# Kernel optimization log

Measured on AMD Instinct MI355X. Metric: run time of the kernel, lower is better.

Reference implementation:

```python
import jax, jax.numpy as jnp
import numpy as np

DIM = 64        # output embedding dim
N_CHUNKS = 3
D = 4           # per-core dim = ceil(DIM ** (1/N_CHUNKS))
RANK = 16
HRANGE = 131072
BATCH = 131072


def setup_inputs() -> dict:
    key = jax.random.key(0)
    k_hs, k_s, k_e, k_c = jax.random.split(key, 4)
    hs = jax.random.randint(k_hs, (BATCH, N_CHUNKS), 0, HRANGE, dtype=jnp.int64)
    # init per reset_parameters (split_dim=True): scale = (d*rank)**-0.5 for cores/end,
    # start_core uniform in +-d**-0.5
    scale = (D * RANK) ** -0.5
    s0 = D ** -0.5
    start_core = jax.random.uniform(k_s, (HRANGE, D, RANK), jnp.float32, -s0, s0)
    end_core = jax.random.uniform(k_e, (HRANGE, D, RANK), jnp.float32, -scale, scale)
    cores = jax.random.uniform(k_c, (N_CHUNKS - 2, HRANGE, D, RANK, RANK), jnp.float32, -scale, scale)
    return {"hs": hs, "start_core": start_core, "end_core": end_core, "cores": cores}


def reference(hs, start_core, end_core, cores):
    B = hs.shape[0]
    # split_dim=True branch of TensorTrainEmbedding.forward
    v = end_core[hs[:, -1]]                      # [B, d, r]
    for i in range(hs.shape[1] - 2):             # fixed small loop over TT cores
        core = cores[i][hs[:, i + 1]]            # [B, d, r, r] irregular gather
        v = jnp.einsum('bdsr,ber->bdes', core, v)  # [B, d, e, r]
        v = v.reshape(B, -1, v.shape[-1])        # flatten(1,2) -> [B, d*e, r]
    v = jnp.einsum('bdr,ber->bde', start_core[hs[:, 0]], v)  # [B, d, e]
    v = v.reshape(B, -1)[:, :DIM]                # [B, dim]
    return v
```

## Files before the change

### kernel.cpp

```cpp
#include <hip/hip_runtime.h>


#define CAP 16
#define WPB 4
#define T_STRIDE 20
#define HRANGE_C 131072

#define WS_COUNTS_OFF 0
#define WS_TABLE_OFF  (HRANGE_C * 4)
#define WS_NEEDED     (HRANGE_C * 4 + HRANGE_C * CAP * 4)

#define WAVE_LDS_FENCE() do { \
    asm volatile("s_waitcnt lgkmcnt(0)" ::: "memory"); \
    __builtin_amdgcn_sched_barrier(0); \
} while (0)

__global__ __launch_bounds__(256) void build_kernel(
    const int* __restrict__ hs, unsigned* __restrict__ counts,
    unsigned* __restrict__ table, int B)
{
    int b = blockIdx.x * 256 + threadIdx.x;
    if (b < B) {
        unsigned h1 = (unsigned)hs[3 * b + 1];
        unsigned slot = atomicAdd(&counts[h1], 1u);
        if (slot < CAP) table[h1 * CAP + slot] = (unsigned)b;
    }
}

__global__ __launch_bounds__(256) void tt_embed_dedup_kernel(
    const int* __restrict__ hs,
    const float* __restrict__ start_core,
    const float* __restrict__ end_core,
    const float* __restrict__ cores,
    const unsigned* __restrict__ counts,
    const unsigned* __restrict__ table,
    float* __restrict__ out)
{
    __shared__ __align__(16) float lds_t[WPB][16 * T_STRIDE];

    const int tid  = threadIdx.x;
    const int wave = tid >> 6;
    const int lane = tid & 63;

    int bin = blockIdx.x * WPB + wave;
    bin = __builtin_amdgcn_readfirstlane(bin);

    int cnt = (int)counts[bin];
    cnt = __builtin_amdgcn_readfirstlane(cnt);
    if (cnt == 0) return;
    if (cnt > CAP) cnt = CAP;

    const float* crp = cores + ((size_t)bin << 10) + lane * 16;
    float c[16];
    *(float4*)(c + 0)  = *(const float4*)(crp + 0);
    *(float4*)(c + 4)  = *(const float4*)(crp + 4);
    *(float4*)(c + 8)  = *(const float4*)(crp + 8);
    *(float4*)(c + 12) = *(const float4*)(crp + 12);

    const int d = lane >> 4;
    const int s = lane & 15;
    float* tw = &lds_t[wave][(d * 4) * T_STRIDE + s];
    const float* tr = &lds_t[wave][(lane & 15) * T_STRIDE];

    for (int j = 0; j < cnt; ++j) {
        int b = (int)table[bin * CAP + j];
        b = __builtin_amdgcn_readfirstlane(b);
        const int h0 = __builtin_amdgcn_readfirstlane(hs[3 * b + 0]);
        const int h2 = __builtin_amdgcn_readfirstlane(hs[3 * b + 2]);

        const float* stp = start_core + ((size_t)h0 << 6) + ((lane >> 4) << 4);
        float st[16];
        *(float4*)(st + 0)  = *(const float4*)(stp + 0);
        *(float4*)(st + 4)  = *(const float4*)(stp + 4);
        *(float4*)(st + 8)  = *(const float4*)(stp + 8);
        *(float4*)(st + 12) = *(const float4*)(stp + 12);

        const float* v0p = end_core + ((size_t)h2 << 6);
        #pragma unroll
        for (int e = 0; e < 4; ++e) {
            const float* ve = v0p + e * 16;
            float a = c[0] * ve[0];
            #pragma unroll
            for (int r = 1; r < 16; ++r)
                a = fmaf(c[r], ve[r], a);
            tw[e * T_STRIDE] = a;
        }

        WAVE_LDS_FENCE();

        float tt[16];
        *(float4*)(tt + 0)  = *(const float4*)(tr + 0);
        *(float4*)(tt + 4)  = *(const float4*)(tr + 4);
        *(float4*)(tt + 8)  = *(const float4*)(tr + 8);
        *(float4*)(tt + 12) = *(const float4*)(tr + 12);

        float a = st[0] * tt[0];
        #pragma unroll
        for (int k = 1; k < 16; ++k)
            a = fmaf(st[k], tt[k], a);

        out[((size_t)b << 6) + lane] = a;

        WAVE_LDS_FENCE();
    }
}

__global__ __launch_bounds__(256) void tt_embed_plain_kernel(
    const int* __restrict__ hs,
    const float* __restrict__ start_core,
    const float* __restrict__ end_core,
    const float* __restrict__ cores,
    float* __restrict__ out,
    int B)
{
    __shared__ __align__(16) float lds_t[WPB][16 * T_STRIDE];
    const int tid  = threadIdx.x;
    const int wave = tid >> 6;
    const int lane = tid & 63;

    int b = blockIdx.x * WPB + wave;
    b = __builtin_amdgcn_readfirstlane(b);
    if (b >= B) return;

    const int h0 = __builtin_amdgcn_readfirstlane(hs[3 * b + 0]);
    const int h1 = __builtin_amdgcn_readfirstlane(hs[3 * b + 1]);
    const int h2 = __builtin_amdgcn_readfirstlane(hs[3 * b + 2]);

    const float* crp = cores + ((size_t)h1 << 10) + lane * 16;
    float c[16];
    *(float4*)(c + 0)  = *(const float4*)(crp + 0);
    *(float4*)(c + 4)  = *(const float4*)(crp + 4);
    *(float4*)(c + 8)  = *(const float4*)(crp + 8);
    *(float4*)(c + 12) = *(const float4*)(crp + 12);

    const float* stp = start_core + ((size_t)h0 << 6) + ((lane >> 4) << 4);
    float st[16];
    *(float4*)(st + 0)  = *(const float4*)(stp + 0);
    *(float4*)(st + 4)  = *(const float4*)(stp + 4);
    *(float4*)(st + 8)  = *(const float4*)(stp + 8);
    *(float4*)(st + 12) = *(const float4*)(stp + 12);

    const float* v0p = end_core + ((size_t)h2 << 6);
    const int d = lane >> 4;
    const int s = lane & 15;
    #pragma unroll
    for (int e = 0; e < 4; ++e) {
        const float* ve = v0p + e * 16;
        float a = c[0] * ve[0];
        #pragma unroll
        for (int r = 1; r < 16; ++r)
            a = fmaf(c[r], ve[r], a);
        lds_t[wave][(d * 4 + e) * T_STRIDE + s] = a;
    }

    WAVE_LDS_FENCE();

    const float* tp = &lds_t[wave][(lane & 15) * T_STRIDE];
    float tt[16];
    *(float4*)(tt + 0)  = *(const float4*)(tp + 0);
    *(float4*)(tt + 4)  = *(const float4*)(tp + 4);
    *(float4*)(tt + 8)  = *(const float4*)(tp + 8);
    *(float4*)(tt + 12) = *(const float4*)(tp + 12);

    float a = st[0] * tt[0];
    #pragma unroll
    for (int k = 1; k < 16; ++k)
        a = fmaf(st[k], tt[k], a);
    out[((size_t)b << 6) + lane] = a;
}

extern "C" void kernel_launch(void* const* d_in, const int* in_sizes, int n_in,
                              void* d_out, int out_size, void* d_ws, size_t ws_size,
                              hipStream_t stream) {
    const int*   hs         = (const int*)d_in[0];
    const float* start_core = (const float*)d_in[1];
    const float* end_core   = (const float*)d_in[2];
    const float* cores      = (const float*)d_in[3];
    float* out = (float*)d_out;

    const int B = in_sizes[0] / 3;

    const bool dedup = (B == HRANGE_C) && (ws_size >= (size_t)WS_NEEDED);

    if (dedup) {
        unsigned* counts = (unsigned*)((char*)d_ws + WS_COUNTS_OFF);
        unsigned* table  = (unsigned*)((char*)d_ws + WS_TABLE_OFF);

        hipMemsetAsync(counts, 0, HRANGE_C * 4, stream);
        hipLaunchKernelGGL(build_kernel, dim3((B + 255) / 256), dim3(256), 0,
                           stream, hs, counts, table, B);
        hipLaunchKernelGGL(tt_embed_dedup_kernel,
                           dim3(HRANGE_C / WPB), dim3(256), 0, stream,
                           hs, start_core, end_core, cores, counts, table, out);
    } else {
        hipLaunchKernelGGL(tt_embed_plain_kernel,
                           dim3((B + WPB - 1) / WPB), dim3(256), 0, stream,
                           hs, start_core, end_core, cores, out, B);
    }
}
```

Baseline: 108.7 us.

## Compact non-empty bins into a worklist and add an overflow path

The build step now stores h0 and h2 next to the batch index in uint4 table entries, so the main kernel no longer rereads hs. A compaction kernel builds a worklist of only the non-empty h1 bins, and a grid-stride main kernel walks that list instead of launching one wave per possible bin, many of which are empty. CAP drops to 8, and entries past it go to an overflow list that a separate small kernel processes, so no rows are silently dropped. The cost is two extra kernel launches and more atomics on shared counters.

```diff
diff --git a/kernel.cpp b/kernel.cpp
--- a/kernel.cpp
+++ b/kernel.cpp
@@ -1,14 +1,19 @@
 #include <hip/hip_runtime.h>
 
 
-#define CAP 16
+#define CAP 8
 #define WPB 4
 #define T_STRIDE 20
 #define HRANGE_C 131072
+#define MAIN_BLOCKS 8192
+#define OVF_BLOCKS 32
 
 #define WS_COUNTS_OFF 0
-#define WS_TABLE_OFF  (HRANGE_C * 4)
-#define WS_NEEDED     (HRANGE_C * 4 + HRANGE_C * CAP * 4)
+#define WS_CTRS_OFF   (HRANGE_C * 4)
+#define WS_WORK_OFF   (1u << 20)
+#define WS_OVF_OFF    ((1u << 20) + (HRANGE_C * 4))
+#define WS_TABLE_OFF  (2u << 20)
+#define WS_NEEDED     ((2u << 20) + (size_t)HRANGE_C * CAP * 16)
 
 #define WAVE_LDS_FENCE() do { \
     asm volatile("s_waitcnt lgkmcnt(0)" ::: "memory"); \
@@ -17,56 +22,146 @@
 
 __global__ __launch_bounds__(256) void build_kernel(
     const int* __restrict__ hs, unsigned* __restrict__ counts,
-    unsigned* __restrict__ table, int B)
+    uint4* __restrict__ table, unsigned* __restrict__ ctrs,
+    unsigned* __restrict__ ovf, int B)
 {
     int b = blockIdx.x * 256 + threadIdx.x;
-    if (b < B) {
-        unsigned h1 = (unsigned)hs[3 * b + 1];
-        unsigned slot = atomicAdd(&counts[h1], 1u);
-        if (slot < CAP) table[h1 * CAP + slot] = (unsigned)b;
-    }
-}
-
-__global__ __launch_bounds__(256) void tt_embed_dedup_kernel(
+    if (b >= B) return;
+    unsigned h0 = (unsigned)hs[3 * b + 0];
+    unsigned h1 = (unsigned)hs[3 * b + 1];
+    unsigned h2 = (unsigned)hs[3 * b + 2];
+    unsigned slot = atomicAdd(&counts[h1], 1u);
+    if (slot < CAP) {
+        table[h1 * CAP + slot] = make_uint4((unsigned)b, h0, h2, 0u);
+    } else {
+        unsigned o = atomicAdd(&ctrs[1], 1u);
+        ovf[o] = (unsigned)b;
+    }
+}
+
+__global__ __launch_bounds__(256) void compact_kernel(
+    const unsigned* __restrict__ counts, unsigned* __restrict__ ctrs,
+    unsigned* __restrict__ worklist)
+{
+    int h = blockIdx.x * 256 + threadIdx.x;
+    unsigned c = counts[h];
+    if (c > 0) {
+        unsigned cc = c > CAP ? (unsigned)CAP : c;
+        unsigned s = atomicAdd(&ctrs[0], 1u);
+        worklist[s] = (unsigned)h | (cc << 20);
+    }
+}
+
+__global__ __launch_bounds__(256) void tt_main_kernel(
+    const float* __restrict__ start_core,
+    const float* __restrict__ end_core,
+    const float* __restrict__ cores,
+    const unsigned* __restrict__ ctrs,
+    const unsigned* __restrict__ worklist,
+    const uint4* __restrict__ table,
+    float* __restrict__ out)
+{
+    __shared__ __align__(16) float lds_t[WPB][16 * T_STRIDE];
+
+    const int tid  = threadIdx.x;
+    const int wave = tid >> 6;
+    const int lane = tid & 63;
+
+    const int n = __builtin_amdgcn_readfirstlane((int)ctrs[0]);
+    const int stride = MAIN_BLOCKS * WPB;
+
+    const int d = lane >> 4;
+    const int s = lane & 15;
+    float* tw = &lds_t[wave][(d * 4) * T_STRIDE + s];
+    const float* tr = &lds_t[wave][(lane & 15) * T_STRIDE];
+
+    for (int i = blockIdx.x * WPB + wave; i < n; i += stride) {
+        const unsigned w = (unsigned)__builtin_amdgcn_readfirstlane(
+                               (int)worklist[i]);
+        const int h1  = (int)(w & 0xFFFFFu);
+        const int cnt = (int)(w >> 20);
+
+        const float* crp = cores + ((size_t)h1 << 10) + lane * 16;
+        float c[16];
+        *(float4*)(c + 0)  = *(const float4*)(crp + 0);
+        *(float4*)(c + 4)  = *(const float4*)(crp + 4);
+        *(float4*)(c + 8)  = *(const float4*)(crp + 8);
+        *(float4*)(c + 12) = *(const float4*)(crp + 12);
+
+        const uint4* ep = table + (size_t)h1 * CAP;
+
+        for (int j = 0; j < cnt; ++j) {
+            const uint4 e = ep[j];
+            const int b  = __builtin_amdgcn_readfirstlane((int)e.x);
+            const int h0 = __builtin_amdgcn_readfirstlane((int)e.y);
+            const int h2 = __builtin_amdgcn_readfirstlane((int)e.z);
+
+            const float* stp = start_core + ((size_t)h0 << 6) + ((lane >> 4) << 4);
+            float st[16];
+            *(float4*)(st + 0)  = *(const float4*)(stp + 0);
+            *(float4*)(st + 4)  = *(const float4*)(stp + 4);
+            *(float4*)(st + 8)  = *(const float4*)(stp + 8);
+            *(float4*)(st + 12) = *(const float4*)(stp + 12);
+
+            const float* v0p = end_core + ((size_t)h2 << 6);
+            #pragma unroll
+            for (int e4 = 0; e4 < 4; ++e4) {
+                const float* ve = v0p + e4 * 16;
+                float a = c[0] * ve[0];
+                #pragma unroll
+                for (int r = 1; r < 16; ++r)
+                    a = fmaf(c[r], ve[r], a);
+                tw[e4 * T_STRIDE] = a;
+            }
+
+            WAVE_LDS_FENCE();
+
+            float tt[16];
+            *(float4*)(tt + 0)  = *(const float4*)(tr + 0);
+            *(float4*)(tt + 4)  = *(const float4*)(tr + 4);
+            *(float4*)(tt + 8)  = *(const float4*)(tr + 8);
+            *(float4*)(tt + 12) = *(const float4*)(tr + 12);
+
+            float a = st[0] * tt[0];
+            #pragma unroll
+            for (int k = 1; k < 16; ++k)
+                a = fmaf(st[k], tt[k], a);
+
+            out[((size_t)b << 6) + lane] = a;
+
+            WAVE_LDS_FENCE();
+        }
+    }
+}
+
+__global__ __launch_bounds__(256) void tt_ovf_kernel(
     const int* __restrict__ hs,
     const float* __restrict__ start_core,
     const float* __restrict__ end_core,
     const float* __restrict__ cores,
-    const unsigned* __restrict__ counts,
-    const unsigned* __restrict__ table,
+    const unsigned* __restrict__ ctrs,
+    const unsigned* __restrict__ ovf,
     float* __restrict__ out)
 {
     __shared__ __align__(16) float lds_t[WPB][16 * T_STRIDE];
-
     const int tid  = threadIdx.x;
     const int wave = tid >> 6;
     const int lane = tid & 63;
 
-    int bin = blockIdx.x * WPB + wave;
-    bin = __builtin_amdgcn_readfirstlane(bin);
-
-    int cnt = (int)counts[bin];
-    cnt = __builtin_amdgcn_readfirstlane(cnt);
-    if (cnt == 0) return;
-    if (cnt > CAP) cnt = CAP;
-
-    const float* crp = cores + ((size_t)bin << 10) + lane * 16;
-    float c[16];
-    *(float4*)(c + 0)  = *(const float4*)(crp + 0);
-    *(float4*)(c + 4)  = *(const float4*)(crp + 4);
-    *(float4*)(c + 8)  = *(const float4*)(crp + 8);
-    *(float4*)(c + 12) = *(const float4*)(crp + 12);
-
-    const int d = lane >> 4;
-    const int s = lane & 15;
-    float* tw = &lds_t[wave][(d * 4) * T_STRIDE + s];
-    const float* tr = &lds_t[wave][(lane & 15) * T_STRIDE];
-
-    for (int j = 0; j < cnt; ++j) {
-        int b = (int)table[bin * CAP + j];
-        b = __builtin_amdgcn_readfirstlane(b);
+    const int nv = __builtin_amdgcn_readfirstlane((int)ctrs[1]);
+
+    for (int k = blockIdx.x * WPB + wave; k < nv; k += OVF_BLOCKS * WPB) {
+        const int b  = __builtin_amdgcn_readfirstlane((int)ovf[k]);
         const int h0 = __builtin_amdgcn_readfirstlane(hs[3 * b + 0]);
+        const int h1 = __builtin_amdgcn_readfirstlane(hs[3 * b + 1]);
         const int h2 = __builtin_amdgcn_readfirstlane(hs[3 * b + 2]);
+
+        const float* crp = cores + ((size_t)h1 << 10) + lane * 16;
+        float c[16];
+        *(float4*)(c + 0)  = *(const float4*)(crp + 0);
+        *(float4*)(c + 4)  = *(const float4*)(crp + 4);
+        *(float4*)(c + 8)  = *(const float4*)(crp + 8);
+        *(float4*)(c + 12) = *(const float4*)(crp + 12);
 
         const float* stp = start_core + ((size_t)h0 << 6) + ((lane >> 4) << 4);
         float st[16];
@@ -76,36 +171,38 @@
         *(float4*)(st + 12) = *(const float4*)(stp + 12);
 
         const float* v0p = end_core + ((size_t)h2 << 6);
+        const int d = lane >> 4;
+        const int s = lane & 15;
         #pragma unroll
-        for (int e = 0; e < 4; ++e) {
-            const float* ve = v0p + e * 16;
+        for (int e4 = 0; e4 < 4; ++e4) {
+            const float* ve = v0p + e4 * 16;
             float a = c[0] * ve[0];
             #pragma unroll
             for (int r = 1; r < 16; ++r)
                 a = fmaf(c[r], ve[r], a);
-            tw[e * T_STRIDE] = a;
+            lds_t[wave][(d * 4 + e4) * T_STRIDE + s] = a;
         }
 
         WAVE_LDS_FENCE();
 
+        const float* tp = &lds_t[wave][(lane & 15) * T_STRIDE];
         float tt[16];
-        *(float4*)(tt + 0)  = *(const float4*)(tr + 0);
-        *(float4*)(tt + 4)  = *(const float4*)(tr + 4);
-        *(float4*)(tt + 8)  = *(const float4*)(tr + 8);
-        *(float4*)(tt + 12) = *(const float4*)(tr + 12);
+        *(float4*)(tt + 0)  = *(const float4*)(tp + 0);
+        *(float4*)(tt + 4)  = *(const float4*)(tp + 4);
+        *(float4*)(tt + 8)  = *(const float4*)(tp + 8);
+        *(float4*)(tt + 12) = *(const float4*)(tp + 12);
 
         float a = st[0] * tt[0];
         #pragma unroll
-        for (int k = 1; k < 16; ++k)
-            a = fmaf(st[k], tt[k], a);
-
+        for (int kk = 1; kk < 16; ++kk)
+            a = fmaf(st[kk], tt[kk], a);
         out[((size_t)b << 6) + lane] = a;
 
         WAVE_LDS_FENCE();
     }
 }
 
-__global__ __launch_bounds__(256) void tt_embed_plain_kernel(
+__global__ __launch_bounds__(256) void tt_plain_kernel(
     const int* __restrict__ hs,
     const float* __restrict__ start_core,
     const float* __restrict__ end_core,
@@ -144,13 +241,13 @@
     const int d = lane >> 4;
     const int s = lane & 15;
     #pragma unroll
-    for (int e = 0; e < 4; ++e) {
-        const float* ve = v0p + e * 16;
+    for (int e4 = 0; e4 < 4; ++e4) {
+        const float* ve = v0p + e4 * 16;
         float a = c[0] * ve[0];
         #pragma unroll
         for (int r = 1; r < 16; ++r)
             a = fmaf(c[r], ve[r], a);
-        lds_t[wave][(d * 4 + e) * T_STRIDE + s] = a;
+        lds_t[wave][(d * 4 + e4) * T_STRIDE + s] = a;
     }
 
     WAVE_LDS_FENCE();
@@ -164,8 +261,8 @@
 
     float a = st[0] * tt[0];
     #pragma unroll
-    for (int k = 1; k < 16; ++k)
-        a = fmaf(st[k], tt[k], a);
+    for (int kk = 1; kk < 16; ++kk)
+        a = fmaf(st[kk], tt[kk], a);
     out[((size_t)b << 6) + lane] = a;
 }
 
@@ -180,21 +277,29 @@
 
     const int B = in_sizes[0] / 3;
 
-    const bool dedup = (B == HRANGE_C) && (ws_size >= (size_t)WS_NEEDED);
+    const bool dedup = (B == HRANGE_C) && (ws_size >= WS_NEEDED);
 
     if (dedup) {
-        unsigned* counts = (unsigned*)((char*)d_ws + WS_COUNTS_OFF);
-        unsigned* table  = (unsigned*)((char*)d_ws + WS_TABLE_OFF);
-
-        hipMemsetAsync(counts, 0, HRANGE_C * 4, stream);
+        unsigned* counts   = (unsigned*)((char*)d_ws + WS_COUNTS_OFF);
+        unsigned* ctrs     = (unsigned*)((char*)d_ws + WS_CTRS_OFF);
+        unsigned* worklist = (unsigned*)((char*)d_ws + WS_WORK_OFF);
+        unsigned* ovf      = (unsigned*)((char*)d_ws + WS_OVF_OFF);
+        uint4*    table    = (uint4*)((char*)d_ws + WS_TABLE_OFF);
+
+        hipMemsetAsync(d_ws, 0, HRANGE_C * 4 + 16, stream);
         hipLaunchKernelGGL(build_kernel, dim3((B + 255) / 256), dim3(256), 0,
-                           stream, hs, counts, table, B);
-        hipLaunchKernelGGL(tt_embed_dedup_kernel,
-                           dim3(HRANGE_C / WPB), dim3(256), 0, stream,
-                           hs, start_core, end_core, cores, counts, table, out);
+                           stream, hs, counts, table, ctrs, ovf, B);
+        hipLaunchKernelGGL(compact_kernel, dim3(HRANGE_C / 256), dim3(256), 0,
+                           stream, counts, ctrs, worklist);
+        hipLaunchKernelGGL(tt_main_kernel, dim3(MAIN_BLOCKS), dim3(256), 0,
+                           stream, start_core, end_core, cores, ctrs, worklist,
+                           table, out);
+        hipLaunchKernelGGL(tt_ovf_kernel, dim3(OVF_BLOCKS), dim3(256), 0,
+                           stream, hs, start_core, end_core, cores, ctrs, ovf,
+                           out);
     } else {
-        hipLaunchKernelGGL(tt_embed_plain_kernel,
-                           dim3((B + WPB - 1) / WPB), dim3(256), 0, stream,
+        hipLaunchKernelGGL(tt_plain_kernel, dim3((B + WPB - 1) / WPB),
+                           dim3(256), 0, stream,
                            hs, start_core, end_core, cores, out, B);
     }
 }
```

Measured after the change: 127.1 us. 16.9% more time.
